# Optimization experiments

Hardware: AMD Instinct MI355X
Metric: run time of the kernel (lower is better)

Reference implementation:

```python
import jax, jax.numpy as jnp
import numpy as np

DT = 0.001
HIDDEN = 512
OUT = 128

def setup_inputs() -> dict:
    key = jax.random.key(0)
    k1, k2 = jax.random.split(key)
    x = jax.random.normal(k1, (64, 2048, HIDDEN), dtype=jnp.float32)
    # torch Linear default init ~ U(-1/sqrt(fan_in), 1/sqrt(fan_in)), weight shape [out, in]
    lim = 1.0 / np.sqrt(HIDDEN)
    W = jax.random.uniform(k2, (OUT, HIDDEN), dtype=jnp.float32, minval=-lim, maxval=lim)
    tau_syn = jnp.asarray(0.5, dtype=jnp.float32)  # tau_syn_out (used as tau_syn_inv)
    tau_mem = jnp.asarray(0.5, dtype=jnp.float32)  # tau_mem_out (used as tau_mem_inv)
    return {"x": x, "W": W, "tau_syn": tau_syn, "tau_mem": tau_mem}

def reference(x, W, tau_syn, tau_mem):
    # SNNDecode.forward: clamp taus, permute to [seq, batch, in], per-step
    # Linear + norse LI (leaky integrator) feed-forward step with v_leak = 0.
    tau_syn = jnp.clip(tau_syn, 0.0, 1.0)
    tau_mem = jnp.clip(tau_mem, 0.0, 1.0)
    batch, seq, _ = x.shape
    # The per-step Linear is recurrence-independent: hoist it into one big GEMM.
    # z_all: [seq, batch, out]
    z_all = jnp.einsum('bsh,oh->sbo', x, W)
    v0 = jnp.zeros((batch, OUT), dtype=x.dtype)
    i0 = jnp.zeros((batch, OUT), dtype=x.dtype)

    def step(carry, z):
        v, i = carry
        # li_feed_forward_step: dv = dt*tau_mem_inv*((v_leak - v) + i)
        v_new = v + DT * tau_mem * (i - v)
        i_dec = i - DT * tau_syn * i
        i_new = i_dec + z
        return (v_new, i_new), v_new

    (v_f, i_f), voltages = jax.lax.scan(step, (v0, i0), z_all)
    # output stacked over time: [seq, batch, out]; final state (v, i)
    return voltages, v_f, i_f
```

## Files before the change

### kernel.cpp

```cpp
#include <hip/hip_runtime.h>
#include <hip/hip_bf16.h>


typedef __attribute__((ext_vector_type(4))) float    f4;
typedef __attribute__((ext_vector_type(2))) float    f2;
typedef __attribute__((ext_vector_type(8))) short    s8;
typedef __attribute__((ext_vector_type(4))) unsigned u4;

#define SEQ    2048
#define HID    512
#define CHAINS 8192
#define VOLT   16777216
#define NCH    32

__device__ __forceinline__ float clamp01(float x) { return fminf(fmaxf(x, 0.f), 1.f); }

__device__ __forceinline__ unsigned pkbf(float x, float y) {
  float2 t; t.x = x; t.y = y;
  union { __hip_bfloat162 h; unsigned u; } c;
  c.h = __float22bfloat162_rn(t);
  return c.u;
}

__device__ __forceinline__ short f2bf(float f) {
  union { float f; unsigned u; } c; c.f = f;
  unsigned u = c.u;
  unsigned r = (u + 0x7fffu + ((u >> 16) & 1u)) >> 16;
  return (short)r;
}

__device__ __forceinline__ int swz(int row, int k) {
  return (row * 64 + k) ^ ((row & 7) << 3);
}

__global__ __launch_bounds__(256) void k_wconv(const float* __restrict__ W,
                                               unsigned short* __restrict__ Wb) {
  const int i = blockIdx.x * 256 + threadIdx.x;
  const f4 lo = ((const f4*)W)[2 * i];
  const f4 hi = ((const f4*)W)[2 * i + 1];
  s8 v;
#pragma unroll
  for (int j = 0; j < 4; ++j) { v[j] = f2bf(lo[j]); v[j + 4] = f2bf(hi[j]); }
  ((s8*)Wb)[i] = v;
}

__global__ __launch_bounds__(256, 2) void k_gemm(const float* __restrict__ X,
                                                 const unsigned short* __restrict__ Wb,
                                                 float* __restrict__ Z,
                                                 const float* __restrict__ tau_syn,
                                                 const float* __restrict__ tau_mem,
                                                 float* __restrict__ ws) {
  __shared__ __align__(16) char smem[65536];
  short* const AS = (short*)smem;
  float* const ZS = (float*)smem;

  const int tid = threadIdx.x;
  const int blk = blockIdx.x;
  const int m0  = blk << 7;
  const int bI  = blk >> 4;
  const int t0  = (blk & 15) << 7;

  const int rbase = tid >> 3;
  const int coff  = (tid & 7) << 3;

  const int lane = tid & 63;
  const int wid  = tid >> 6;
  const int wmb  = (wid >> 1) << 6;
  const int wnb  = (wid & 1) << 6;
  const int lr   = lane & 15;
  const int lk   = (lane >> 4) << 3;

  const float* pX[4];
#pragma unroll
  for (int c = 0; c < 4; ++c)
    pX[c] = X + (size_t)(m0 + (c << 5) + rbase) * HID + coff;
  const unsigned short* pB[4];
#pragma unroll
  for (int ni = 0; ni < 4; ++ni)
    pB[ni] = Wb + (size_t)(wnb + (ni << 4) + lr) * HID + lk;

  f4 acc[4][4];
#pragma unroll
  for (int mi = 0; mi < 4; ++mi)
#pragma unroll
    for (int ni = 0; ni < 4; ++ni) acc[mi][ni] = (f4){0.f, 0.f, 0.f, 0.f};

  f4 xa[3][4][2];
#pragma unroll
  for (int c = 0; c < 4; ++c) {
    xa[0][c][0] = *(const f4*)(pX[c]);
    xa[0][c][1] = *(const f4*)(pX[c] + 4);
    xa[1][c][0] = *(const f4*)(pX[c] + 64);
    xa[1][c][1] = *(const f4*)(pX[c] + 68);
  }

#pragma unroll
  for (int ks = 0; ks < 8; ++ks) {
    const int cur = ks % 3;
    short* const Ac = AS + ((ks & 1) << 13);
#pragma unroll
    for (int c = 0; c < 4; ++c) {
      const int row = (c << 5) + rbase;
      u4 va;
      va[0] = pkbf(xa[cur][c][0][0], xa[cur][c][0][1]);
      va[1] = pkbf(xa[cur][c][0][2], xa[cur][c][0][3]);
      va[2] = pkbf(xa[cur][c][1][0], xa[cur][c][1][1]);
      va[3] = pkbf(xa[cur][c][1][2], xa[cur][c][1][3]);
      *(u4*)&Ac[swz(row, coff)] = va;
    }
    __syncthreads();
    s8 bg[2][4];
#pragma unroll
    for (int kk = 0; kk < 2; ++kk)
#pragma unroll
      for (int ni = 0; ni < 4; ++ni)
        bg[kk][ni] = *(const s8*)(pB[ni] + (ks << 6) + (kk << 5));
    if (ks < 6) {
      const int k0 = (ks + 2) << 6;
      const int nxt = (ks + 2) % 3;
#pragma unroll
      for (int c = 0; c < 4; ++c) {
        xa[nxt][c][0] = *(const f4*)(pX[c] + k0);
        xa[nxt][c][1] = *(const f4*)(pX[c] + k0 + 4);
      }
    }
#pragma unroll
    for (int kk = 0; kk < 2; ++kk) {
      s8 af[4];
#pragma unroll
      for (int mi = 0; mi < 4; ++mi)
        af[mi] = *(const s8*)&Ac[swz(wmb + (mi << 4) + lr, (kk << 5) + lk)];
#pragma unroll
      for (int mi = 0; mi < 4; ++mi)
#pragma unroll
        for (int ni = 0; ni < 4; ++ni)
          acc[mi][ni] = __builtin_amdgcn_mfma_f32_16x16x32_bf16(af[mi], bg[kk][ni],
                                                                acc[mi][ni], 0, 0, 0);
    }
  }

  __syncthreads();
  const int rr = (lane >> 4) << 2;
#pragma unroll
  for (int mi = 0; mi < 4; ++mi)
#pragma unroll
    for (int ni = 0; ni < 4; ++ni)
#pragma unroll
      for (int r = 0; r < 4; ++r)
        ZS[(wmb + (mi << 4) + rr + r) * 128 + wnb + (ni << 4) + lr] = acc[mi][ni][r];
  __syncthreads();

  {
    float* const Zrow = Z + (size_t)t0 * 8192 + (bI << 7);
#pragma unroll
    for (int i = 0; i < 16; ++i) {
      const int idx  = (i << 8) + tid;
      const int toff = idx >> 5;
      const int c4   = idx & 31;
      *(f4*)(Zrow + (size_t)toff * 8192 + (c4 << 2)) = *(const f4*)&ZS[toff * 128 + (c4 << 2)];
    }
  }
  {
    const float a  = 0.001f * clamp01(tau_mem[0]);
    const float eb = 1.f - 0.001f * clamp01(tau_syn[0]);
    const int h = tid >> 7, col = tid & 127;
    const float* zs = ZS + ((h << 6) * 128) + col;
    float v = 0.f, ii = 0.f;
#pragma unroll 8
    for (int j = 0; j < 64; ++j) {
      const float z = zs[j * 128];
      v  = v + a * (ii - v);
      ii = eb * ii + z;
    }
    const int q     = ((blk & 15) << 1) + h;
    const int chain = (bI << 7) + col;
    ws[q * CHAINS + chain]                 = v;
    ws[NCH * CHAINS + q * CHAINS + chain]  = ii;
  }
}

__global__ __launch_bounds__(256) void k_combine(const float* __restrict__ tau_syn,
                                                 const float* __restrict__ tau_mem,
                                                 float* __restrict__ Out,
                                                 float* __restrict__ ws) {
  const int c = blockIdx.x * 256 + threadIdx.x;
  const float a  = 0.001f * clamp01(tau_mem[0]);
  const float bb = 0.001f * clamp01(tau_syn[0]);
  const float ea = 1.f - a, eb = 1.f - bb;
  float P = 1.f, Q = 0.f, R = 1.f;
#pragma unroll
  for (int j = 0; j < 64; ++j) { float Pn = P * ea; Q = P * a + Q * eb; P = Pn; R *= eb; }
  float* vend = ws;
  float* iend = ws + NCH * CHAINS;
  float sv = 0.f, si = 0.f;
  for (int q = 0; q < NCH; ++q) {
    const int idx = q * CHAINS + c;
    const float ve = vend[idx], ie = iend[idx];
    vend[idx] = sv;  iend[idx] = si;
    const float nv = P * sv + Q * si + ve;
    si = R * si + ie;
    sv = nv;
  }
  Out[VOLT + c] = sv;
  Out[VOLT + CHAINS + c] = si;
}

__global__ __launch_bounds__(256) void k_emit(const float* __restrict__ tau_syn,
                                              const float* __restrict__ tau_mem,
                                              float* Z,
                                              const float* __restrict__ ws) {
  const int tid = threadIdx.x;
  const int cg = (blockIdx.x & 63) * 64 + (tid & 63);
  const int q  = (blockIdx.x >> 6) * 4 + (tid >> 6);
  const float a  = 0.001f * clamp01(tau_mem[0]);
  const float eb = 1.f - 0.001f * clamp01(tau_syn[0]);
  f2* z2 = (f2*)Z;
  const f2* vin = (const f2*)ws;
  const f2* iin = vin + NCH * 4096;
  f2 v  = vin[q * 4096 + cg];
  f2 ii = iin[q * 4096 + cg];
  const int tb = q << 6;
#pragma unroll 8
  for (int j = 0; j < 64; ++j) {
    const size_t idx = (size_t)(tb + j) * 4096 + cg;
    f2 z = z2[idx];
    v  = v + a * (ii - v);
    z2[idx] = v;
    ii = eb * ii + z;
  }
}

extern "C" void kernel_launch(void* const* d_in, const int* in_sizes, int n_in,
                              void* d_out, int out_size, void* d_ws, size_t ws_size,
                              hipStream_t stream) {
  const float* X   = (const float*)d_in[0];
  const float* W   = (const float*)d_in[1];
  const float* tsy = (const float*)d_in[2];
  const float* tme = (const float*)d_in[3];
  float* Out = (float*)d_out;
  float* ws  = (float*)d_ws;
  unsigned short* Wb = (unsigned short*)((char*)d_ws + (2u << 20));

  k_wconv<<<32, 256, 0, stream>>>(W, Wb);
  k_gemm<<<1024, 256, 0, stream>>>(X, Wb, Out, tsy, tme, ws);
  k_combine<<<32, 256, 0, stream>>>(tsy, tme, Out, ws);
  k_emit<<<512, 256, 0, stream>>>(tsy, tme, Out, ws);
}
```

Measured before the change: 104.6 us.

## Fold chunk-prefix combine into emit kernel with 32-step chunks

Removes the serial k_combine kernel. Each emit thread now recomputes the prefix state for its chunk by scanning all earlier chunk end-states itself. Chunks are halved to 32 steps (64 chunks), and emit uses f4 vectors over more time blocks, which shortens the serial recurrence per thread. This saves one launch and a serial pass, at the cost of redundant prefix work (up to 63 iterations of loads per thread) and uneven work across blocks.

```diff
diff --git a/kernel.cpp b/kernel.cpp
--- a/kernel.cpp
+++ b/kernel.cpp
@@ -3,7 +3,6 @@
 
 
 typedef __attribute__((ext_vector_type(4))) float    f4;
-typedef __attribute__((ext_vector_type(2))) float    f2;
 typedef __attribute__((ext_vector_type(8))) short    s8;
 typedef __attribute__((ext_vector_type(4))) unsigned u4;
 
@@ -11,7 +10,8 @@
 #define HID    512
 #define CHAINS 8192
 #define VOLT   16777216
-#define NCH    32
+#define NCH    64
+#define CHUNK  32
 
 __device__ __forceinline__ float clamp01(float x) { return fminf(fmaxf(x, 0.f), 1.f); }
 
@@ -163,46 +163,24 @@
   {
     const float a  = 0.001f * clamp01(tau_mem[0]);
     const float eb = 1.f - 0.001f * clamp01(tau_syn[0]);
-    const int h = tid >> 7, col = tid & 127;
-    const float* zs = ZS + ((h << 6) * 128) + col;
-    float v = 0.f, ii = 0.f;
+    const int col = tid & 127, h = tid >> 7;
+    const int chain = (bI << 7) + col;
+#pragma unroll
+    for (int s = 0; s < 2; ++s) {
+      const int r0 = (h << 6) + (s << 5);
+      const float* zs = ZS + r0 * 128 + col;
+      float v = 0.f, ii = 0.f;
 #pragma unroll 8
-    for (int j = 0; j < 64; ++j) {
-      const float z = zs[j * 128];
-      v  = v + a * (ii - v);
-      ii = eb * ii + z;
-    }
-    const int q     = ((blk & 15) << 1) + h;
-    const int chain = (bI << 7) + col;
-    ws[q * CHAINS + chain]                 = v;
-    ws[NCH * CHAINS + q * CHAINS + chain]  = ii;
-  }
-}
-
-__global__ __launch_bounds__(256) void k_combine(const float* __restrict__ tau_syn,
-                                                 const float* __restrict__ tau_mem,
-                                                 float* __restrict__ Out,
-                                                 float* __restrict__ ws) {
-  const int c = blockIdx.x * 256 + threadIdx.x;
-  const float a  = 0.001f * clamp01(tau_mem[0]);
-  const float bb = 0.001f * clamp01(tau_syn[0]);
-  const float ea = 1.f - a, eb = 1.f - bb;
-  float P = 1.f, Q = 0.f, R = 1.f;
-#pragma unroll
-  for (int j = 0; j < 64; ++j) { float Pn = P * ea; Q = P * a + Q * eb; P = Pn; R *= eb; }
-  float* vend = ws;
-  float* iend = ws + NCH * CHAINS;
-  float sv = 0.f, si = 0.f;
-  for (int q = 0; q < NCH; ++q) {
-    const int idx = q * CHAINS + c;
-    const float ve = vend[idx], ie = iend[idx];
-    vend[idx] = sv;  iend[idx] = si;
-    const float nv = P * sv + Q * si + ve;
-    si = R * si + ie;
-    sv = nv;
-  }
-  Out[VOLT + c] = sv;
-  Out[VOLT + CHAINS + c] = si;
+      for (int j = 0; j < CHUNK; ++j) {
+        const float z = zs[j * 128];
+        v  = v + a * (ii - v);
+        ii = eb * ii + z;
+      }
+      const int q = ((blk & 15) << 2) + (h << 1) + s;
+      ws[q * CHAINS + chain]                 = v;
+      ws[NCH * CHAINS + q * CHAINS + chain]  = ii;
+    }
+  }
 }
 
 __global__ __launch_bounds__(256) void k_emit(const float* __restrict__ tau_syn,
@@ -210,23 +188,41 @@
                                               float* Z,
                                               const float* __restrict__ ws) {
   const int tid = threadIdx.x;
-  const int cg = (blockIdx.x & 63) * 64 + (tid & 63);
-  const int q  = (blockIdx.x >> 6) * 4 + (tid >> 6);
+  const int cg = (blockIdx.x & 31) * 64 + (tid & 63);
+  const int q  = (blockIdx.x >> 5) * 4 + (tid >> 6);
   const float a  = 0.001f * clamp01(tau_mem[0]);
-  const float eb = 1.f - 0.001f * clamp01(tau_syn[0]);
-  f2* z2 = (f2*)Z;
-  const f2* vin = (const f2*)ws;
-  const f2* iin = vin + NCH * 4096;
-  f2 v  = vin[q * 4096 + cg];
-  f2 ii = iin[q * 4096 + cg];
-  const int tb = q << 6;
+  const float bb = 0.001f * clamp01(tau_syn[0]);
+  const float ea = 1.f - a, eb = 1.f - bb;
+  float P = 1.f, Q = 0.f, R = 1.f;
+#pragma unroll
+  for (int j = 0; j < CHUNK; ++j) { float Pn = P * ea; Q = P * a + Q * eb; P = Pn; R *= eb; }
+
+  const f4* vend = (const f4*)ws;
+  const f4* iend = vend + NCH * 2048;
+  f4 sv = (f4){0.f, 0.f, 0.f, 0.f}, si = (f4){0.f, 0.f, 0.f, 0.f};
+#pragma unroll 4
+  for (int p = 0; p < q; ++p) {
+    const f4 ve = vend[p * 2048 + cg];
+    const f4 ie = iend[p * 2048 + cg];
+    const f4 nv = P * sv + Q * si + ve;
+    si = R * si + ie;
+    sv = nv;
+  }
+
+  f4* z4 = (f4*)Z;
+  const int tb = q << 5;
+  f4 v = sv, ii = si;
 #pragma unroll 8
-  for (int j = 0; j < 64; ++j) {
-    const size_t idx = (size_t)(tb + j) * 4096 + cg;
-    f2 z = z2[idx];
+  for (int j = 0; j < CHUNK; ++j) {
+    const size_t idx = (size_t)(tb + j) * 2048 + cg;
+    f4 z = z4[idx];
     v  = v + a * (ii - v);
-    z2[idx] = v;
+    z4[idx] = v;
     ii = eb * ii + z;
+  }
+  if (q == NCH - 1) {
+    ((f4*)(Z + VOLT))[cg]        = v;
+    ((f4*)(Z + VOLT + CHAINS))[cg] = ii;
   }
 }
 
@@ -239,10 +235,9 @@
   const float* tme = (const float*)d_in[3];
   float* Out = (float*)d_out;
   float* ws  = (float*)d_ws;
-  unsigned short* Wb = (unsigned short*)((char*)d_ws + (2u << 20));
+  unsigned short* Wb = (unsigned short*)((char*)d_ws + (4u << 20));
 
   k_wconv<<<32, 256, 0, stream>>>(W, Wb);
   k_gemm<<<1024, 256, 0, stream>>>(X, Wb, Out, tsy, tme, ws);
-  k_combine<<<32, 256, 0, stream>>>(tsy, tme, Out, ws);
   k_emit<<<512, 256, 0, stream>>>(tsy, tme, Out, ws);
 }
```

Result: no change. 104.8 us (+0.1%).

## Scan each 128-step tile fully in GEMM epilogue and fix up with a linear correction

Applied to the files above, without the earlier changes.

The GEMM epilogue now runs the local leaky-integrator scan inside shared memory and stitches its two 64-step halves, writing voltages (not raw z) to the output. A small combine kernel propagates carries across 16 tiles. A fix-up kernel then adds a precomputed linear response (alpha*v_in + beta*i_in) to tiles 1-15. This replaces the read-modify-write emit pass over z with a read-modify-write pass that needs no serial recurrence. The combine kernel runs only 8 blocks, and the epilogue gets a serial correction loop.

```diff
diff --git a/kernel.cpp b/kernel.cpp
--- a/kernel.cpp
+++ b/kernel.cpp
@@ -3,7 +3,6 @@
 
 
 typedef __attribute__((ext_vector_type(4))) float    f4;
-typedef __attribute__((ext_vector_type(2))) float    f2;
 typedef __attribute__((ext_vector_type(8))) short    s8;
 typedef __attribute__((ext_vector_type(4))) unsigned u4;
 
@@ -11,7 +10,7 @@
 #define HID    512
 #define CHAINS 8192
 #define VOLT   16777216
-#define NCH    32
+#define NT     16
 
 __device__ __forceinline__ float clamp01(float x) { return fminf(fmaxf(x, 0.f), 1.f); }
 
@@ -46,11 +45,12 @@
 
 __global__ __launch_bounds__(256, 2) void k_gemm(const float* __restrict__ X,
                                                  const unsigned short* __restrict__ Wb,
-                                                 float* __restrict__ Z,
+                                                 float* __restrict__ Out,
                                                  const float* __restrict__ tau_syn,
                                                  const float* __restrict__ tau_mem,
                                                  float* __restrict__ ws) {
   __shared__ __align__(16) char smem[65536];
+  __shared__ float vh0[128], ih0[128];
   short* const AS = (short*)smem;
   float* const ZS = (float*)smem;
 
@@ -58,7 +58,8 @@
   const int blk = blockIdx.x;
   const int m0  = blk << 7;
   const int bI  = blk >> 4;
-  const int t0  = (blk & 15) << 7;
+  const int jt  = blk & 15;
+  const int t0  = jt << 7;
 
   const int rbase = tid >> 3;
   const int coff  = (tid & 7) << 3;
@@ -150,83 +151,116 @@
         ZS[(wmb + (mi << 4) + rr + r) * 128 + wnb + (ni << 4) + lr] = acc[mi][ni][r];
   __syncthreads();
 
+  const float a  = 0.001f * clamp01(tau_mem[0]);
+  const float bb = 0.001f * clamp01(tau_syn[0]);
+  const float ea = 1.f - a, eb = 1.f - bb;
+  const int h = tid >> 7, col = tid & 127;
+
   {
-    float* const Zrow = Z + (size_t)t0 * 8192 + (bI << 7);
+    float* zc = ZS + ((h << 6) * 128) + col;
+    float v = 0.f, ii = 0.f;
+#pragma unroll 8
+    for (int j = 0; j < 64; ++j) {
+      const float z = zc[j * 128];
+      v  = v + a * (ii - v);
+      zc[j * 128] = v;
+      ii = eb * ii + z;
+    }
+    if (h == 0) { vh0[col] = v; ih0[col] = ii; }
+    __syncthreads();
+    if (h == 1) {
+      const float v0 = vh0[col], i0 = ih0[col];
+      float al = 1.f, be = 0.f, ep = 1.f;
+      float* zc1 = ZS + (64 * 128) + col;
+      for (int j = 0; j < 64; ++j) {
+        const float aln = al * ea;
+        be = al * a + be * eb;
+        al = aln;
+        ep *= eb;
+        zc1[j * 128] += al * v0 + be * i0;
+      }
+      const float vE = v + al * v0 + be * i0;
+      const float iE = ii + ep * i0;
+      ws[jt * CHAINS + (bI << 7) + col]                = vE;
+      ws[NT * CHAINS + jt * CHAINS + (bI << 7) + col]  = iE;
+    }
+  }
+  __syncthreads();
+
+  {
+    float* const Orow = Out + (size_t)t0 * 8192 + (bI << 7);
 #pragma unroll
     for (int i = 0; i < 16; ++i) {
       const int idx  = (i << 8) + tid;
       const int toff = idx >> 5;
       const int c4   = idx & 31;
-      *(f4*)(Zrow + (size_t)toff * 8192 + (c4 << 2)) = *(const f4*)&ZS[toff * 128 + (c4 << 2)];
-    }
-  }
-  {
-    const float a  = 0.001f * clamp01(tau_mem[0]);
-    const float eb = 1.f - 0.001f * clamp01(tau_syn[0]);
-    const int h = tid >> 7, col = tid & 127;
-    const float* zs = ZS + ((h << 6) * 128) + col;
-    float v = 0.f, ii = 0.f;
-#pragma unroll 8
-    for (int j = 0; j < 64; ++j) {
-      const float z = zs[j * 128];
-      v  = v + a * (ii - v);
-      ii = eb * ii + z;
-    }
-    const int q     = ((blk & 15) << 1) + h;
-    const int chain = (bI << 7) + col;
-    ws[q * CHAINS + chain]                 = v;
-    ws[NCH * CHAINS + q * CHAINS + chain]  = ii;
-  }
-}
-
-__global__ __launch_bounds__(256) void k_combine(const float* __restrict__ tau_syn,
-                                                 const float* __restrict__ tau_mem,
-                                                 float* __restrict__ Out,
-                                                 float* __restrict__ ws) {
-  const int c = blockIdx.x * 256 + threadIdx.x;
+      *(f4*)(Orow + (size_t)toff * 8192 + (c4 << 2)) = *(const f4*)&ZS[toff * 128 + (c4 << 2)];
+    }
+  }
+}
+
+__global__ __launch_bounds__(256) void k_tilecombine(const float* __restrict__ tau_syn,
+                                                     const float* __restrict__ tau_mem,
+                                                     float* __restrict__ Out,
+                                                     float* __restrict__ ws) {
+  const int cg = blockIdx.x * 256 + threadIdx.x;
   const float a  = 0.001f * clamp01(tau_mem[0]);
   const float bb = 0.001f * clamp01(tau_syn[0]);
   const float ea = 1.f - a, eb = 1.f - bb;
   float P = 1.f, Q = 0.f, R = 1.f;
 #pragma unroll
-  for (int j = 0; j < 64; ++j) { float Pn = P * ea; Q = P * a + Q * eb; P = Pn; R *= eb; }
-  float* vend = ws;
-  float* iend = ws + NCH * CHAINS;
-  float sv = 0.f, si = 0.f;
-  for (int q = 0; q < NCH; ++q) {
-    const int idx = q * CHAINS + c;
-    const float ve = vend[idx], ie = iend[idx];
-    vend[idx] = sv;  iend[idx] = si;
-    const float nv = P * sv + Q * si + ve;
-    si = R * si + ie;
+  for (int j = 0; j < 128; ++j) { const float Pn = P * ea; Q = P * a + Q * eb; P = Pn; R *= eb; }
+
+  const f4* vT = (const f4*)ws;
+  const f4* iT = vT + NT * 2048;
+  f4* vin = (f4*)ws + 2 * NT * 2048;
+  f4* iin = vin + NT * 2048;
+  f4 sv = (f4){0.f, 0.f, 0.f, 0.f}, si = (f4){0.f, 0.f, 0.f, 0.f};
+  for (int p = 0; p < NT; ++p) {
+    vin[p * 2048 + cg] = sv;  iin[p * 2048 + cg] = si;
+    const f4 Ev = vT[p * 2048 + cg], Ei = iT[p * 2048 + cg];
+    const f4 nv = P * sv + Q * si + Ev;
+    si = R * si + Ei;
     sv = nv;
   }
-  Out[VOLT + c] = sv;
-  Out[VOLT + CHAINS + c] = si;
-}
-
-__global__ __launch_bounds__(256) void k_emit(const float* __restrict__ tau_syn,
-                                              const float* __restrict__ tau_mem,
-                                              float* Z,
-                                              const float* __restrict__ ws) {
+  ((f4*)(Out + VOLT))[cg]          = sv;
+  ((f4*)(Out + VOLT + CHAINS))[cg] = si;
+}
+
+__global__ __launch_bounds__(256) void k_fix(const float* __restrict__ tau_syn,
+                                             const float* __restrict__ tau_mem,
+                                             float* __restrict__ Out,
+                                             const float* __restrict__ ws) {
+  __shared__ float tA[128], tB[128];
   const int tid = threadIdx.x;
-  const int cg = (blockIdx.x & 63) * 64 + (tid & 63);
-  const int q  = (blockIdx.x >> 6) * 4 + (tid >> 6);
-  const float a  = 0.001f * clamp01(tau_mem[0]);
-  const float eb = 1.f - 0.001f * clamp01(tau_syn[0]);
-  f2* z2 = (f2*)Z;
-  const f2* vin = (const f2*)ws;
-  const f2* iin = vin + NCH * 4096;
-  f2 v  = vin[q * 4096 + cg];
-  f2 ii = iin[q * 4096 + cg];
-  const int tb = q << 6;
-#pragma unroll 8
-  for (int j = 0; j < 64; ++j) {
-    const size_t idx = (size_t)(tb + j) * 4096 + cg;
-    f2 z = z2[idx];
-    v  = v + a * (ii - v);
-    z2[idx] = v;
-    ii = eb * ii + z;
+  if (tid == 0) {
+    const float a  = 0.001f * clamp01(tau_mem[0]);
+    const float bb = 0.001f * clamp01(tau_syn[0]);
+    const float ea = 1.f - a, eb = 1.f - bb;
+    float al = 1.f, be = 0.f, ep = 1.f;
+    for (int j = 0; j < 128; ++j) {
+      const float aln = al * ea;
+      be = al * a + be * eb;
+      al = aln;
+      ep *= eb;
+      tA[j] = al; tB[j] = be;
+    }
+  }
+  __syncthreads();
+  const f4* vin = (const f4*)ws + 2 * NT * 2048;
+  const f4* iin = vin + NT * 2048;
+  f4* o4 = (f4*)Out;
+  const int N = 15 << 18;
+  for (int g = blockIdx.x * 256 + tid; g < N; g += 2048 * 256) {
+    const int tile = 1 + (g >> 18);
+    const int r    = g & ((1 << 18) - 1);
+    const int j    = r >> 11;
+    const int c4   = r & 2047;
+    const f4 vi = vin[tile * 2048 + c4];
+    const f4 ij = iin[tile * 2048 + c4];
+    const float A = tA[j], B = tB[j];
+    const size_t t = ((size_t)((tile << 7) + j)) * 2048 + c4;
+    o4[t] = o4[t] + A * vi + B * ij;
   }
 }
 
@@ -243,6 +277,6 @@
 
   k_wconv<<<32, 256, 0, stream>>>(W, Wb);
   k_gemm<<<1024, 256, 0, stream>>>(X, Wb, Out, tsy, tme, ws);
-  k_combine<<<32, 256, 0, stream>>>(tsy, tme, Out, ws);
-  k_emit<<<512, 256, 0, stream>>>(tsy, tme, Out, ws);
-}
+  k_tilecombine<<<8, 256, 0, stream>>>(tsy, tme, Out, ws);
+  k_fix<<<2048, 256, 0, stream>>>(tsy, tme, Out, ws);
+}
```

Measured after the change: 110.8 us. 1.06x slower.
